# Performance work log

Measured on AMD Instinct MI355X. Metric: run time of the kernel, lower is better.

The kernel has to match this reference:

```python
import jax, jax.numpy as jnp
import numpy as np

N, E, G = 50000, 800000, 512
DIN, H, DOUT, L = 128, 256, 128, 5
H4 = 4 * H


def _ffnn(h, W1, b1, W2, b2):
    # Linear -> exact GELU (torch default) -> Linear
    return jax.nn.gelu(h @ W1 + b1, approximate=False) @ W2 + b2


def _mean_pool(h, batch):
    s = jax.ops.segment_sum(h, batch, num_segments=G)
    c = jax.ops.segment_sum(jnp.ones((h.shape[0], 1), h.dtype), batch, num_segments=G)
    return s / jnp.maximum(c, 1.0)


def setup_inputs() -> dict:
    key = jax.random.key(0)
    ks = iter(jax.random.split(key, 64))
    w = lambda *s: jax.random.normal(next(ks), s, jnp.float32) * 0.02
    z = lambda *s: jnp.zeros(s, jnp.float32)
    inp = {
        'x': jax.random.normal(next(ks), (N, DIN), jnp.float32),
        'edge_index': jax.random.randint(next(ks), (2, E), 0, N, jnp.int32),
        'batch': jnp.sort(jax.random.randint(next(ks), (N,), 0, G, jnp.int32)),
        'pre_W1': w(DIN, H), 'pre_b1': z(H), 'pre_W2': w(H, H), 'pre_b2': z(H),
        'gin_W1': w(L, H, H), 'gin_b1': z(L, H), 'gin_W2': w(L, H, H), 'gin_b2': z(L, H),
        'ffn_W1': w(L, H, H), 'ffn_b1': z(L, H), 'ffn_W2': w(L, H, H), 'ffn_b2': z(L, H),
        'upd_W1': w(L, H, H), 'upd_b1': z(L, H), 'upd_W2': w(L, H, H4), 'upd_b2': z(L, H4),
        'prop_W1': w(L, H4, H), 'prop_b1': z(L, H), 'prop_W2': w(L, H, H), 'prop_b2': z(L, H),
        'bn_gamma': jnp.ones((L, H), jnp.float32), 'bn_beta': z(L, H),
        'vn': jax.random.normal(next(ks), (1, H4), jnp.float32),
        'post_W1': w(H, H), 'post_b1': z(H), 'post_W2': w(H, DOUT), 'post_b2': z(DOUT),
    }
    return inp


def reference(x, edge_index, batch,
              pre_W1, pre_b1, pre_W2, pre_b2,
              gin_W1, gin_b1, gin_W2, gin_b2,
              ffn_W1, ffn_b1, ffn_W2, ffn_b2,
              upd_W1, upd_b1, upd_W2, upd_b2,
              prop_W1, prop_b1, prop_W2, prop_b2,
              bn_gamma, bn_beta, vn,
              post_W1, post_b1, post_W2, post_b2):
    src, dst = edge_index[0], edge_index[1]
    h = _ffnn(x, pre_W1, pre_b1, pre_W2, pre_b2)
    for i in range(L):
        # virtual node update and propagation
        v = vn + _ffnn(_mean_pool(h, batch), upd_W1[i], upd_b1[i], upd_W2[i], upd_b2[i])  # [G, 4H]
        outvn = _ffnn(v, prop_W1[i], prop_b1[i], prop_W2[i], prop_b2[i])  # [G, H]
        # GINConv (eps=0): nn((1+eps)*h + sum_{j->i} h_j), residual
        agg = jax.ops.segment_sum(h[src], dst, num_segments=N)
        h = _ffnn(h + agg, gin_W1[i], gin_b1[i], gin_W2[i], gin_b2[i]) + h
        # BatchNorm1d (batch statistics, biased var)
        mu = jnp.mean(h, axis=0)
        var = jnp.mean((h - mu) ** 2, axis=0)
        h = (h - mu) * jax.lax.rsqrt(var + 1e-5) * bn_gamma[i] + bn_beta[i]
        # broadcast VN to nodes, FFNN with residual (dropout = identity in eval)
        h = _ffnn(outvn[batch] + h, ffn_W1[i], ffn_b1[i], ffn_W2[i], ffn_b2[i]) + h
    out = _ffnn(_mean_pool(h, batch), post_W1, post_b1, post_W2, post_b2)
    return out
```

## Files before the change

### kernel.cpp

```cpp
#include <hip/hip_runtime.h>
#include <hip/hip_bf16.h>
#include <math.h>

#define NN 50000
#define NNP 50048
#define NE 800000
#define NG 512
#define DIN 128
#define HD 256
#define DOUT 128
#define NL 5
#define H4 1024

typedef _Float16 f16x8 __attribute__((ext_vector_type(8)));
typedef _Float16 f16x4 __attribute__((ext_vector_type(4)));
typedef float f32x4 __attribute__((ext_vector_type(4)));

__device__ __forceinline__ float gelu_exact(float x) {
    return 0.5f * x * (1.0f + erff(x * 0.70710678118654752f));
}

__device__ __forceinline__ void gl_lds16(const _Float16* g, _Float16* l) {
    __builtin_amdgcn_global_load_lds(
        (const __attribute__((address_space(1))) unsigned int*)g,
        (__attribute__((address_space(3))) unsigned int*)l, 16, 0, 0);
}

__global__ void k_hist(const int* __restrict__ idx, int* __restrict__ cnt, int n) {
    int i = blockIdx.x * blockDim.x + threadIdx.x;
    if (i < n) atomicAdd(&cnt[idx[i]], 1);
}

__global__ void k_scan_small(const int* __restrict__ in, int* __restrict__ out, int n) {
    __shared__ int buf[1024];
    int t = threadIdx.x;
    int v = (t < n) ? in[t] : 0;
    buf[t] = v;
    __syncthreads();
    for (int off = 1; off < 1024; off <<= 1) {
        int x = (t >= off) ? buf[t - off] : 0;
        __syncthreads();
        buf[t] += x;
        __syncthreads();
    }
    if (t < n) out[t] = buf[t] - v;
    if (t == 1023) out[n] = buf[1023];
}

__global__ void k_scan_part(const int* __restrict__ in, int* __restrict__ bsum, int n) {
    __shared__ int buf[256];
    int i = blockIdx.x * 256 + threadIdx.x;
    buf[threadIdx.x] = (i < n) ? in[i] : 0;
    __syncthreads();
    for (int off = 128; off > 0; off >>= 1) {
        if (threadIdx.x < off) buf[threadIdx.x] += buf[threadIdx.x + off];
        __syncthreads();
    }
    if (threadIdx.x == 0) bsum[blockIdx.x] = buf[0];
}

__global__ void k_scan_mid(const int* __restrict__ bsum, int* __restrict__ bexcl, int nb,
                           int* __restrict__ out, int n) {
    __shared__ int buf[1024];
    int t = threadIdx.x;
    int v = (t < nb) ? bsum[t] : 0;
    buf[t] = v;
    __syncthreads();
    for (int off = 1; off < 1024; off <<= 1) {
        int x = (t >= off) ? buf[t - off] : 0;
        __syncthreads();
        buf[t] += x;
        __syncthreads();
    }
    if (t < nb) bexcl[t] = buf[t] - v;
    if (t == 1023) out[n] = buf[1023];
}

__global__ void k_scan_out(const int* __restrict__ in, const int* __restrict__ bexcl,
                           int* __restrict__ out, int n) {
    __shared__ int buf[256];
    int i = blockIdx.x * 256 + threadIdx.x;
    int t = threadIdx.x;
    int v = (i < n) ? in[i] : 0;
    buf[t] = v;
    __syncthreads();
    for (int off = 1; off < 256; off <<= 1) {
        int x = (t >= off) ? buf[t - off] : 0;
        __syncthreads();
        buf[t] += x;
        __syncthreads();
    }
    if (i < n) out[i] = bexcl[blockIdx.x] + buf[t] - v;
}

__global__ void k_fill_csr(const int* __restrict__ src, const int* __restrict__ dst,
                           const int* __restrict__ eoff, int* __restrict__ cursor,
                           int* __restrict__ csr, int n) {
    int e = blockIdx.x * blockDim.x + threadIdx.x;
    if (e < n) {
        int d = dst[e];
        int p = atomicAdd(&cursor[d], 1);
        csr[eoff[d] + p] = src[e];
    }
}

__global__ void k_cvt16(const float* __restrict__ in, _Float16* __restrict__ out, int n4) {
    int i = blockIdx.x * blockDim.x + threadIdx.x;
    if (i < n4) {
        float4 v = *(const float4*)&in[i * 4];
        f16x4 o = { (_Float16)v.x, (_Float16)v.y, (_Float16)v.z, (_Float16)v.w };
        *(f16x4*)&out[i * 4] = o;
    }
}

#define NWTJOBS 44
struct WtJobs {
    const float* src[NWTJOBS];
    _Float16* dst[NWTJOBS];
    short K32[NWTJOBS];
    short N32[NWTJOBS];
    short pre[NWTJOBS + 1];
};
__global__ void k_wtb(WtJobs j) {
    int bid = blockIdx.x;
    int lo = 0;
    while (j.pre[lo + 1] <= bid) ++lo;
    int tl = bid - j.pre[lo];
    int nx = j.N32[lo];
    int n0 = (tl % nx) * 32, k0 = (tl / nx) * 32;
    int K = j.K32[lo] * 32, N = nx * 32;
    const float* W = j.src[lo];
    _Float16* Wt = j.dst[lo];
    __shared__ float tile[32][33];
    for (int i = threadIdx.y; i < 32; i += 8)
        tile[i][threadIdx.x] = W[(size_t)(k0 + i) * N + n0 + threadIdx.x];
    __syncthreads();
    for (int i = threadIdx.y; i < 32; i += 8)
        Wt[(size_t)(n0 + i) * K + k0 + threadIdx.x] = (_Float16)tile[threadIdx.x][i];
}

__global__ void k_pool16(const _Float16* __restrict__ h16, const int* __restrict__ goff,
                         _Float16* __restrict__ pool) {
    int g = blockIdx.x;
    int c = threadIdx.x;
    int s = goff[g], e = goff[g + 1];
    float acc = 0.f;
    for (int r = s; r < e; ++r) acc += (float)h16[(size_t)r * HD + c];
    int cnt = e - s;
    pool[g * HD + c] = (_Float16)(acc / (float)(cnt > 0 ? cnt : 1));
}

__global__ __launch_bounds__(256) void k_agg16(const _Float16* __restrict__ h16,
                                               const int* __restrict__ eoff,
                                               const int* __restrict__ csr,
                                               _Float16* __restrict__ out) {
    int node = blockIdx.x * 4 + (threadIdx.x >> 6);
    int lane = threadIdx.x & 63;
    int half = lane >> 5, l = lane & 31;
    f16x8 mine = *(const f16x8*)&h16[(size_t)node * HD + l * 8];
    float acc[8];
#pragma unroll
    for (int q = 0; q < 8; ++q) acc[q] = half ? 0.f : (float)mine[q];
    int s = eoff[node], e = eoff[node + 1];
    for (int base = s; base < e; base += 64) {
        int myi = base + lane;
        int vidx = (myi < e) ? csr[myi] : 0;
        int cnt = min(64, e - base);
        int jj = 0;
        for (; jj + 7 < cnt; jj += 8) {
            int s0 = __shfl(vidx, jj + half);
            int s1 = __shfl(vidx, jj + 2 + half);
            int s2 = __shfl(vidx, jj + 4 + half);
            int s3 = __shfl(vidx, jj + 6 + half);
            f16x8 v0 = *(const f16x8*)&h16[(size_t)s0 * HD + l * 8];
            f16x8 v1 = *(const f16x8*)&h16[(size_t)s1 * HD + l * 8];
            f16x8 v2 = *(const f16x8*)&h16[(size_t)s2 * HD + l * 8];
            f16x8 v3 = *(const f16x8*)&h16[(size_t)s3 * HD + l * 8];
#pragma unroll
            for (int q = 0; q < 8; ++q)
                acc[q] += ((float)v0[q] + (float)v1[q]) + ((float)v2[q] + (float)v3[q]);
        }
        for (; jj + 3 < cnt; jj += 4) {
            int s0 = __shfl(vidx, jj + half);
            int s1 = __shfl(vidx, jj + 2 + half);
            f16x8 v0 = *(const f16x8*)&h16[(size_t)s0 * HD + l * 8];
            f16x8 v1 = *(const f16x8*)&h16[(size_t)s1 * HD + l * 8];
#pragma unroll
            for (int q = 0; q < 8; ++q) acc[q] += (float)v0[q] + (float)v1[q];
        }
        for (; jj < cnt; jj += 2) {
            int i0 = jj + half;
            int s0 = __shfl(vidx, i0);
            if (i0 < cnt) {
                f16x8 v0 = *(const f16x8*)&h16[(size_t)s0 * HD + l * 8];
#pragma unroll
                for (int q = 0; q < 8; ++q) acc[q] += (float)v0[q];
            }
        }
    }
#pragma unroll
    for (int q = 0; q < 8; ++q) acc[q] += __shfl_xor(acc[q], 32);
    if (!half) {
        f16x8 o;
#pragma unroll
        for (int q = 0; q < 8; ++q) o[q] = (_Float16)acc[q];
        *(f16x8*)&out[(size_t)node * HD + l * 8] = o;
    }
}

__global__ void k_bn_final(float* __restrict__ stat,
                           const float* __restrict__ gamma, const float* __restrict__ beta,
                           float* __restrict__ scale, float* __restrict__ shift) {
    int c = threadIdx.x;
    float mu = stat[c] * (1.0f / NN);
    float var = stat[HD + c] * (1.0f / NN) - mu * mu;
    float rs = rsqrtf(var + 1e-5f);
    float sc = rs * gamma[c];
    scale[c] = sc;
    shift[c] = beta[c] - mu * sc;
    stat[c] = 0.f;
    stat[HD + c] = 0.f;
}

template <bool ABN1, bool RES2, bool RESBN2, bool STATS2>
__global__ __launch_bounds__(512) void k_b2b(const _Float16* __restrict__ A16,
                                             const _Float16* __restrict__ G16,
                                             const _Float16* __restrict__ W1t,
                                             const float* __restrict__ b1,
                                             const _Float16* __restrict__ W2t,
                                             const float* __restrict__ b2,
                                             const _Float16* __restrict__ R16,
                                             const float* __restrict__ bnsc,
                                             const float* __restrict__ bnsh,
                                             const float* __restrict__ ovn,
                                             const int* __restrict__ batchv,
                                             float* __restrict__ stat,
                                             _Float16* __restrict__ C16,
                                             int M, int K1) {
    __shared__ _Float16 AC[32][64][8];
    __shared__ _Float16 Bs[2][4][256][8];
    const int t = threadIdx.x;
    const int w = t >> 6, lane = t & 63;
    const int m0 = blockIdx.x * 64;
    const int kb = lane >> 4, fr = lane & 15, rr = lane >> 4;

    auto stageB = [&](int buf, int k0, const _Float16* Wt, int KB) {
        int s0 = t, s1 = t + 512;
        gl_lds16(Wt + (size_t)(s0 & 255) * KB + k0 + (s0 >> 8) * 8, &Bs[buf][s0 >> 8][s0 & 255][0]);
        gl_lds16(Wt + (size_t)(s1 & 255) * KB + k0 + (s1 >> 8) * 8, &Bs[buf][s1 >> 8][s1 & 255][0]);
    };

    const int nchunk = K1 * 8;
    if constexpr (ABN1) {
        for (int c = t; c < nchunk; c += 512) {
            int kblk = c >> 6, row = c & 63;
            int b0 = batchv[min(m0 + row, M - 1)];
            const int c0 = kblk * 8;
            f16x8 g = *(const f16x8*)&G16[(size_t)(m0 + row) * HD + c0];
            f16x8 r0;
#pragma unroll
            for (int q = 0; q < 8; ++q)
                r0[q] = (_Float16)((float)g[q] * bnsc[c0 + q] + bnsh[c0 + q] +
                                   ovn[(size_t)b0 * HD + c0 + q]);
            *(f16x8*)&AC[kblk][row][0] = r0;
        }
    } else {
        for (int c = t; c < nchunk; c += 512) {
            int kblk = c >> 6, row = c & 63;
            gl_lds16(A16 + (size_t)(m0 + row) * K1 + kblk * 8, &AC[kblk][row][0]);
        }
    }
    stageB(0, 0, W1t, K1);
    __syncthreads();

    f32x4 acc1[4][2];
#pragma unroll
    for (int mi = 0; mi < 4; ++mi)
#pragma unroll
        for (int ni = 0; ni < 2; ++ni) acc1[mi][ni] = (f32x4){0.f, 0.f, 0.f, 0.f};

    const int nt1 = K1 >> 5;
    for (int tt = 0; tt < nt1; ++tt) {
        const int cur = tt & 1;
        if (tt + 1 < nt1) stageB(cur ^ 1, (tt + 1) << 5, W1t, K1);
        f16x8 af[4], bf[2];
#pragma unroll
        for (int mi = 0; mi < 4; ++mi)
            af[mi] = *(const f16x8*)&AC[(tt << 2) + kb][mi * 16 + fr][0];
#pragma unroll
        for (int ni = 0; ni < 2; ++ni)
            bf[ni] = *(const f16x8*)&Bs[cur][kb][w * 32 + ni * 16 + fr][0];
#pragma unroll
        for (int mi = 0; mi < 4; ++mi)
#pragma unroll
            for (int ni = 0; ni < 2; ++ni)
                acc1[mi][ni] = __builtin_amdgcn_mfma_f32_16x16x32_f16(af[mi], bf[ni], acc1[mi][ni], 0, 0, 0);
        __syncthreads();
    }

    stageB(0, 0, W2t, HD);
#pragma unroll
    for (int mi = 0; mi < 4; ++mi) {
#pragma unroll
        for (int reg = 0; reg < 4; ++reg) {
            int ml = mi * 16 + rr * 4 + reg;
#pragma unroll
            for (int ni = 0; ni < 2; ++ni) {
                int n = w * 32 + ni * 16 + fr;
                float v = gelu_exact(acc1[mi][ni][reg] + b1[n]);
                AC[n >> 3][ml][n & 7] = (_Float16)v;
            }
        }
    }
    __syncthreads();

    f32x4 acc2[4][2];
#pragma unroll
    for (int mi = 0; mi < 4; ++mi)
#pragma unroll
        for (int ni = 0; ni < 2; ++ni) acc2[mi][ni] = (f32x4){0.f, 0.f, 0.f, 0.f};

    for (int tt = 0; tt < 8; ++tt) {
        const int cur = tt & 1;
        if (tt + 1 < 8) stageB(cur ^ 1, (tt + 1) << 5, W2t, HD);
        f16x8 af[4], bf[2];
#pragma unroll
        for (int mi = 0; mi < 4; ++mi)
            af[mi] = *(const f16x8*)&AC[tt * 4 + kb][mi * 16 + fr][0];
#pragma unroll
        for (int ni = 0; ni < 2; ++ni)
            bf[ni] = *(const f16x8*)&Bs[cur][kb][w * 32 + ni * 16 + fr][0];
#pragma unroll
        for (int mi = 0; mi < 4; ++mi)
#pragma unroll
            for (int ni = 0; ni < 2; ++ni)
                acc2[mi][ni] = __builtin_amdgcn_mfma_f32_16x16x32_f16(af[mi], bf[ni], acc2[mi][ni], 0, 0, 0);
        __syncthreads();
    }

    float cs[2] = {0.f, 0.f}, cq[2] = {0.f, 0.f};
#pragma unroll
    for (int mi = 0; mi < 4; ++mi) {
#pragma unroll
        for (int reg = 0; reg < 4; ++reg) {
            int m = m0 + mi * 16 + rr * 4 + reg;
            if (m < M) {
#pragma unroll
                for (int ni = 0; ni < 2; ++ni) {
                    int n = w * 32 + ni * 16 + fr;
                    float v = acc2[mi][ni][reg] + b2[n];
                    if (RES2) v += (float)R16[(size_t)m * HD + n];
                    if (RESBN2) v += (float)R16[(size_t)m * HD + n] * bnsc[n] + bnsh[n];
                    _Float16 vh = (_Float16)v;
                    C16[(size_t)m * HD + n] = vh;
                    if (STATS2) { float vr = (float)vh; cs[ni] += vr; cq[ni] += vr * vr; }
                }
            }
        }
    }
    if constexpr (STATS2) {
#pragma unroll
        for (int ni = 0; ni < 2; ++ni) {
            cs[ni] += __shfl_xor(cs[ni], 16); cs[ni] += __shfl_xor(cs[ni], 32);
            cq[ni] += __shfl_xor(cq[ni], 16); cq[ni] += __shfl_xor(cq[ni], 32);
        }
        if (lane < 16) {
#pragma unroll
            for (int ni = 0; ni < 2; ++ni) {
                int n = w * 32 + ni * 16 + lane;
                atomicAdd(&stat[n], cs[ni]);
                atomicAdd(&stat[HD + n], cq[ni]);
            }
        }
    }
}

template <bool GELU, bool BIAS2, bool O32, bool O16>
__global__ __launch_bounds__(256) void k_mgemm(const _Float16* __restrict__ A,
                                               const _Float16* __restrict__ Wt,
                                               const float* __restrict__ bias,
                                               const float* __restrict__ bias2,
                                               float* __restrict__ C32,
                                               _Float16* __restrict__ C16,
                                               int M, int N, int K) {
    __shared__ _Float16 As[2][4][64][8];
    __shared__ _Float16 Bs[2][4][128][8];
    const int t = threadIdx.x;
    const int w = t >> 6, lane = t & 63;
    const int m0 = blockIdx.y * 64, n0 = blockIdx.x * 128;
    const int kb = lane >> 4, fr = lane & 15;

    f32x4 acc[4][2];
#pragma unroll
    for (int mi = 0; mi < 4; ++mi)
#pragma unroll
        for (int ni = 0; ni < 2; ++ni) acc[mi][ni] = (f32x4){0.f, 0.f, 0.f, 0.f};

    const _Float16* gA0 = A + (size_t)(m0 + lane) * K + w * 8;
    const _Float16* gB0 = Wt + (size_t)(n0 + lane) * K + w * 8;
    const _Float16* gB1 = Wt + (size_t)(n0 + 64 + lane) * K + w * 8;

    auto stage = [&](int buf, int k0) {
        gl_lds16(gB0 + k0, &Bs[buf][w][0][0]);
        gl_lds16(gB1 + k0, &Bs[buf][w][64][0]);
        gl_lds16(gA0 + k0, &As[buf][w][0][0]);
    };

    const int nt = K >> 5;
    stage(0, 0);
    __syncthreads();
    for (int tt = 0; tt < nt; ++tt) {
        const int cur = tt & 1;
        if (tt + 1 < nt) stage(cur ^ 1, (tt + 1) << 5);
        f16x8 af[4], bf[2];
#pragma unroll
        for (int mi = 0; mi < 4; ++mi)
            af[mi] = *(const f16x8*)&As[cur][kb][mi * 16 + fr][0];
#pragma unroll
        for (int ni = 0; ni < 2; ++ni)
            bf[ni] = *(const f16x8*)&Bs[cur][kb][w * 32 + ni * 16 + fr][0];
#pragma unroll
        for (int mi = 0; mi < 4; ++mi)
#pragma unroll
            for (int ni = 0; ni < 2; ++ni)
                acc[mi][ni] = __builtin_amdgcn_mfma_f32_16x16x32_f16(af[mi], bf[ni], acc[mi][ni], 0, 0, 0);
        __syncthreads();
    }

    const int rr = lane >> 4;
#pragma unroll
    for (int mi = 0; mi < 4; ++mi) {
#pragma unroll
        for (int reg = 0; reg < 4; ++reg) {
            int m = m0 + mi * 16 + rr * 4 + reg;
            if (m < M) {
#pragma unroll
                for (int ni = 0; ni < 2; ++ni) {
                    int n = n0 + w * 32 + ni * 16 + fr;
                    float v = acc[mi][ni][reg] + bias[n];
                    if (BIAS2) v += bias2[n];
                    if (GELU) v = gelu_exact(v);
                    if (O32) C32[(size_t)m * N + n] = v;
                    if (O16) C16[(size_t)m * N + n] = (_Float16)v;
                }
            }
        }
    }
}

static inline void mg_gelu(hipStream_t st, const _Float16* A, const _Float16* Wt,
                           const float* bias, _Float16* C16, int M, int N, int K) {
    dim3 g(N / 128, (M + 63) / 64), b(256);
    k_mgemm<true, false, false, true><<<g, b, 0, st>>>(A, Wt, bias, nullptr, nullptr, C16, M, N, K);
}
static inline void mg_bias2_16(hipStream_t st, const _Float16* A, const _Float16* Wt,
                               const float* bias, const float* bias2, _Float16* C16,
                               int M, int N, int K) {
    dim3 g(N / 128, (M + 63) / 64), b(256);
    k_mgemm<false, true, false, true><<<g, b, 0, st>>>(A, Wt, bias, bias2, nullptr, C16, M, N, K);
}
static inline void mg_f32only(hipStream_t st, const _Float16* A, const _Float16* Wt,
                              const float* bias, float* C32, int M, int N, int K) {
    dim3 g(N / 128, (M + 63) / 64), b(256);
    k_mgemm<false, false, true, false><<<g, b, 0, st>>>(A, Wt, bias, nullptr, C32, nullptr, M, N, K);
}

extern "C" void kernel_launch(void* const* d_in, const int* in_sizes, int n_in,
                              void* d_out, int out_size, void* d_ws, size_t ws_size,
                              hipStream_t stream) {
    const float* x       = (const float*)d_in[0];
    const int*   ei      = (const int*)d_in[1];
    const int*   batch   = (const int*)d_in[2];
    const float* pre_W1  = (const float*)d_in[3];
    const float* pre_b1  = (const float*)d_in[4];
    const float* pre_W2  = (const float*)d_in[5];
    const float* pre_b2  = (const float*)d_in[6];
    const float* gin_W1  = (const float*)d_in[7];
    const float* gin_b1  = (const float*)d_in[8];
    const float* gin_W2  = (const float*)d_in[9];
    const float* gin_b2  = (const float*)d_in[10];
    const float* ffn_W1  = (const float*)d_in[11];
    const float* ffn_b1  = (const float*)d_in[12];
    const float* ffn_W2  = (const float*)d_in[13];
    const float* ffn_b2  = (const float*)d_in[14];
    const float* upd_W1  = (const float*)d_in[15];
    const float* upd_b1  = (const float*)d_in[16];
    const float* upd_W2  = (const float*)d_in[17];
    const float* upd_b2  = (const float*)d_in[18];
    const float* prop_W1 = (const float*)d_in[19];
    const float* prop_b1 = (const float*)d_in[20];
    const float* prop_W2 = (const float*)d_in[21];
    const float* prop_b2 = (const float*)d_in[22];
    const float* bn_gamma= (const float*)d_in[23];
    const float* bn_beta = (const float*)d_in[24];
    const float* vn      = (const float*)d_in[25];
    const float* post_W1 = (const float*)d_in[26];
    const float* post_b1 = (const float*)d_in[27];
    const float* post_W2 = (const float*)d_in[28];
    const float* post_b2 = (const float*)d_in[29];
    float* out = (float*)d_out;

    const int* e_src = ei;
    const int* e_dst = ei + NE;

    char* p = (char*)d_ws;
    auto alloc = [&](size_t bytes) -> char* {
        char* r = p;
        p += (bytes + 255) & ~(size_t)255;
        return r;
    };
    _Float16* h16    = (_Float16*)alloc((size_t)NNP * HD * 2);
    _Float16* g16    = (_Float16*)alloc((size_t)NNP * HD * 2);
    _Float16* t16a   = (_Float16*)alloc((size_t)NNP * HD * 2);
    _Float16* pool16 = (_Float16*)alloc((size_t)NG * HD * 2);
    _Float16* u16    = (_Float16*)alloc((size_t)NG * HD * 2);
    _Float16* vb16   = (_Float16*)alloc((size_t)NG * H4 * 2);
    _Float16* p16    = (_Float16*)alloc((size_t)NG * HD * 2);
    float*    outvn32= (float*)alloc((size_t)NG * HD * 4);
    float*    bnstat = (float*)alloc(2 * HD * 4);
    float*    bnscale= (float*)alloc(HD * 4);
    float*    bnshift= (float*)alloc(HD * 4);
    _Float16* preW1t = (_Float16*)alloc((size_t)HD * DIN * 2);
    _Float16* preW2t = (_Float16*)alloc((size_t)HD * HD * 2);
    _Float16* ginW1t = (_Float16*)alloc((size_t)NL * HD * HD * 2);
    _Float16* ginW2t = (_Float16*)alloc((size_t)NL * HD * HD * 2);
    _Float16* ffnW1t = (_Float16*)alloc((size_t)NL * HD * HD * 2);
    _Float16* ffnW2t = (_Float16*)alloc((size_t)NL * HD * HD * 2);
    _Float16* updW1t = (_Float16*)alloc((size_t)NL * HD * HD * 2);
    _Float16* updW2t = (_Float16*)alloc((size_t)NL * HD * H4 * 2);
    _Float16* propW1t= (_Float16*)alloc((size_t)NL * H4 * HD * 2);
    _Float16* propW2t= (_Float16*)alloc((size_t)NL * HD * HD * 2);
    _Float16* postW1t= (_Float16*)alloc((size_t)HD * HD * 2);
    _Float16* postW2t= (_Float16*)alloc((size_t)DOUT * HD * 2);
    int* gcount = (int*)alloc(NG * 4);
    int* goff   = (int*)alloc((NG + 1) * 4);
    int* deg    = (int*)alloc(NN * 4);
    int* eoff   = (int*)alloc((NN + 1) * 4);
    int* cursor = (int*)alloc(NN * 4);
    int* csr    = (int*)alloc((size_t)NE * 4);
    int* bsum   = (int*)alloc(1024 * 4);
    int* bexcl  = (int*)alloc(1024 * 4);
    _Float16* x16 = t16a;

    {
        size_t span = (size_t)((char*)(cursor + NN) - (char*)gcount);
        hipMemsetAsync(gcount, 0, span, stream);
        hipMemsetAsync(bnstat, 0, 2 * HD * 4, stream);
    }
    hipLaunchKernelGGL(k_hist, dim3((NN + 255) / 256), dim3(256), 0, stream, batch, gcount, NN);
    hipLaunchKernelGGL(k_hist, dim3((NE + 255) / 256), dim3(256), 0, stream, e_dst, deg, NE);
    hipLaunchKernelGGL(k_scan_small, dim3(1), dim3(1024), 0, stream, gcount, goff, NG);
    {
        int nbN = (NN + 255) / 256;
        hipLaunchKernelGGL(k_scan_part, dim3(nbN), dim3(256), 0, stream, deg, bsum, NN);
        hipLaunchKernelGGL(k_scan_mid, dim3(1), dim3(1024), 0, stream, bsum, bexcl, nbN, eoff, NN);
        hipLaunchKernelGGL(k_scan_out, dim3(nbN), dim3(256), 0, stream, deg, bexcl, eoff, NN);
    }
    hipLaunchKernelGGL(k_fill_csr, dim3((NE + 255) / 256), dim3(256), 0, stream, e_src, e_dst, eoff, cursor, csr, NE);

    {
        WtJobs j;
        int idx = 0, tiles = 0;
        auto add = [&](const float* s, _Float16* d, int K, int N) {
            j.src[idx] = s; j.dst[idx] = d;
            j.K32[idx] = (short)(K / 32); j.N32[idx] = (short)(N / 32);
            j.pre[idx] = (short)tiles;
            tiles += (K / 32) * (N / 32);
            ++idx;
        };
        add(pre_W1, preW1t, DIN, HD);
        add(pre_W2, preW2t, HD, HD);
        add(post_W1, postW1t, HD, HD);
        add(post_W2, postW2t, HD, DOUT);
        for (int i = 0; i < NL; ++i) {
            add(gin_W1 + (size_t)i * HD * HD, ginW1t + (size_t)i * HD * HD, HD, HD);
            add(gin_W2 + (size_t)i * HD * HD, ginW2t + (size_t)i * HD * HD, HD, HD);
            add(ffn_W1 + (size_t)i * HD * HD, ffnW1t + (size_t)i * HD * HD, HD, HD);
            add(ffn_W2 + (size_t)i * HD * HD, ffnW2t + (size_t)i * HD * HD, HD, HD);
            add(upd_W1 + (size_t)i * HD * HD, updW1t + (size_t)i * HD * HD, HD, HD);
            add(upd_W2 + (size_t)i * HD * H4, updW2t + (size_t)i * HD * H4, HD, H4);
            add(prop_W1 + (size_t)i * H4 * HD, propW1t + (size_t)i * H4 * HD, H4, HD);
            add(prop_W2 + (size_t)i * HD * HD, propW2t + (size_t)i * HD * HD, HD, HD);
        }
        j.pre[idx] = (short)tiles;
        hipLaunchKernelGGL(k_wtb, dim3(tiles), dim3(32, 8), 0, stream, j);
    }

    int n4 = NN * DIN / 4;
    hipLaunchKernelGGL(k_cvt16, dim3((n4 + 255) / 256), dim3(256), 0, stream, x, x16, n4);

    const int nb2b = NNP / 64;

    hipLaunchKernelGGL((k_b2b<false, false, false, false>), dim3(nb2b), dim3(512), 0, stream,
                       x16, nullptr, preW1t, pre_b1, preW2t, pre_b2,
                       nullptr, nullptr, nullptr, nullptr, nullptr, nullptr,
                       h16, NN, DIN);

    for (int i = 0; i < NL; ++i) {
        const _Float16* uW1 = updW1t + (size_t)i * HD * HD;
        const _Float16* uW2 = updW2t + (size_t)i * HD * H4;
        const _Float16* pW1 = propW1t + (size_t)i * H4 * HD;
        const _Float16* pW2 = propW2t + (size_t)i * HD * HD;

        hipLaunchKernelGGL(k_pool16, dim3(NG), dim3(HD), 0, stream, h16, goff, pool16);
        mg_gelu(stream, pool16, uW1, upd_b1 + (size_t)i * HD, u16, NG, HD, HD);
        mg_bias2_16(stream, u16, uW2, upd_b2 + (size_t)i * H4, vn, vb16, NG, H4, HD);
        mg_gelu(stream, vb16, pW1, prop_b1 + (size_t)i * HD, p16, NG, HD, H4);
        mg_f32only(stream, p16, pW2, prop_b2 + (size_t)i * HD, outvn32, NG, HD, HD);

        hipLaunchKernelGGL(k_agg16, dim3(NN / 4), dim3(256), 0, stream, h16, eoff, csr, t16a);
        hipLaunchKernelGGL((k_b2b<false, true, false, true>), dim3(nb2b), dim3(512), 0, stream,
                           t16a, nullptr,
                           ginW1t + (size_t)i * HD * HD, gin_b1 + (size_t)i * HD,
                           ginW2t + (size_t)i * HD * HD, gin_b2 + (size_t)i * HD,
                           h16, nullptr, nullptr, nullptr, nullptr, bnstat,
                           g16, NN, HD);

        hipLaunchKernelGGL(k_bn_final, dim3(1), dim3(HD), 0, stream, bnstat,
                           bn_gamma + (size_t)i * HD, bn_beta + (size_t)i * HD, bnscale, bnshift);

        hipLaunchKernelGGL((k_b2b<true, false, true, false>), dim3(nb2b), dim3(512), 0, stream,
                           nullptr, g16,
                           ffnW1t + (size_t)i * HD * HD, ffn_b1 + (size_t)i * HD,
                           ffnW2t + (size_t)i * HD * HD, ffn_b2 + (size_t)i * HD,
                           g16, bnscale, bnshift, outvn32, batch, nullptr,
                           h16, NN, HD);
    }

    hipLaunchKernelGGL(k_pool16, dim3(NG), dim3(HD), 0, stream, h16, goff, pool16);
    mg_gelu(stream, pool16, postW1t, post_b1, u16, NG, HD, HD);
    mg_f32only(stream, u16, postW2t, post_b2, out, NG, DOUT, HD);
}
```

Baseline: 1.674 ms.

## Triple-buffer weight staging across both GEMMs with one barrier per step

```diff
diff --git a/kernel.cpp b/kernel.cpp
--- a/kernel.cpp
+++ b/kernel.cpp
@@ -222,7 +222,7 @@
     stat[HD + c] = 0.f;
 }
 
-template <bool ABN1, bool RES2, bool RESBN2, bool STATS2>
+template <bool ABN1, bool RES2, bool RESBN2, bool STATS2, int K1>
 __global__ __launch_bounds__(512) void k_b2b(const _Float16* __restrict__ A16,
                                              const _Float16* __restrict__ G16,
                                              const _Float16* __restrict__ W1t,
@@ -236,23 +236,32 @@
                                              const int* __restrict__ batchv,
                                              float* __restrict__ stat,
                                              _Float16* __restrict__ C16,
-                                             int M, int K1) {
+                                             int M) {
     __shared__ _Float16 AC[32][64][8];
-    __shared__ _Float16 Bs[2][4][256][8];
+    __shared__ _Float16 Bs[3][4][256][8];
+    constexpr int NT1 = K1 >> 5;
+    constexpr int NSTEP = NT1 + 8;
     const int t = threadIdx.x;
     const int w = t >> 6, lane = t & 63;
     const int m0 = blockIdx.x * 64;
     const int kb = lane >> 4, fr = lane & 15, rr = lane >> 4;
 
-    auto stageB = [&](int buf, int k0, const _Float16* Wt, int KB) {
+    auto stageB = [&](int s) {
+        const _Float16* Wt = (s < NT1) ? W1t : W2t;
+        const int KB = (s < NT1) ? K1 : HD;
+        const int k0 = ((s < NT1) ? s : (s - NT1)) << 5;
+        const int buf = s % 3;
         int s0 = t, s1 = t + 512;
         gl_lds16(Wt + (size_t)(s0 & 255) * KB + k0 + (s0 >> 8) * 8, &Bs[buf][s0 >> 8][s0 & 255][0]);
         gl_lds16(Wt + (size_t)(s1 & 255) * KB + k0 + (s1 >> 8) * 8, &Bs[buf][s1 >> 8][s1 & 255][0]);
     };
 
-    const int nchunk = K1 * 8;
+    float b1r[2];
+#pragma unroll
+    for (int ni = 0; ni < 2; ++ni) b1r[ni] = b1[w * 32 + ni * 16 + fr];
+
     if constexpr (ABN1) {
-        for (int c = t; c < nchunk; c += 512) {
+        for (int c = t; c < K1 * 8; c += 512) {
             int kblk = c >> 6, row = c & 63;
             int b0 = batchv[min(m0 + row, M - 1)];
             const int c0 = kblk * 8;
@@ -265,13 +274,15 @@
             *(f16x8*)&AC[kblk][row][0] = r0;
         }
     } else {
-        for (int c = t; c < nchunk; c += 512) {
+        for (int c = t; c < K1 * 8; c += 512) {
             int kblk = c >> 6, row = c & 63;
             gl_lds16(A16 + (size_t)(m0 + row) * K1 + kblk * 8, &AC[kblk][row][0]);
         }
     }
-    stageB(0, 0, W1t, K1);
-    __syncthreads();
+    stageB(0);
+    stageB(1);
+    asm volatile("s_waitcnt vmcnt(2) lgkmcnt(0)" ::: "memory");
+    __builtin_amdgcn_s_barrier();
 
     f32x4 acc1[4][2];
 #pragma unroll
@@ -279,26 +290,29 @@
 #pragma unroll
         for (int ni = 0; ni < 2; ++ni) acc1[mi][ni] = (f32x4){0.f, 0.f, 0.f, 0.f};
 
-    const int nt1 = K1 >> 5;
-    for (int tt = 0; tt < nt1; ++tt) {
-        const int cur = tt & 1;
-        if (tt + 1 < nt1) stageB(cur ^ 1, (tt + 1) << 5, W1t, K1);
+#pragma unroll
+    for (int s = 0; s < NT1; ++s) {
+        if (s) {
+            asm volatile("s_waitcnt vmcnt(2)" ::: "memory");
+            __builtin_amdgcn_s_barrier();
+        }
         f16x8 af[4], bf[2];
 #pragma unroll
         for (int mi = 0; mi < 4; ++mi)
-            af[mi] = *(const f16x8*)&AC[(tt << 2) + kb][mi * 16 + fr][0];
+            af[mi] = *(const f16x8*)&AC[(s << 2) + kb][mi * 16 + fr][0];
 #pragma unroll
         for (int ni = 0; ni < 2; ++ni)
-            bf[ni] = *(const f16x8*)&Bs[cur][kb][w * 32 + ni * 16 + fr][0];
+            bf[ni] = *(const f16x8*)&Bs[s % 3][kb][w * 32 + ni * 16 + fr][0];
+        stageB(s + 2);
 #pragma unroll
         for (int mi = 0; mi < 4; ++mi)
 #pragma unroll
             for (int ni = 0; ni < 2; ++ni)
                 acc1[mi][ni] = __builtin_amdgcn_mfma_f32_16x16x32_f16(af[mi], bf[ni], acc1[mi][ni], 0, 0, 0);
-        __syncthreads();
-    }
-
-    stageB(0, 0, W2t, HD);
+    }
+
+    asm volatile("s_waitcnt vmcnt(2)" ::: "memory");
+    __builtin_amdgcn_s_barrier();
 #pragma unroll
     for (int mi = 0; mi < 4; ++mi) {
 #pragma unroll
@@ -307,12 +321,13 @@
 #pragma unroll
             for (int ni = 0; ni < 2; ++ni) {
                 int n = w * 32 + ni * 16 + fr;
-                float v = gelu_exact(acc1[mi][ni][reg] + b1[n]);
+                float v = gelu_exact(acc1[mi][ni][reg] + b1r[ni]);
                 AC[n >> 3][ml][n & 7] = (_Float16)v;
             }
         }
     }
-    __syncthreads();
+    asm volatile("s_waitcnt lgkmcnt(0)" ::: "memory");
+    __builtin_amdgcn_s_barrier();
 
     f32x4 acc2[4][2];
 #pragma unroll
@@ -320,22 +335,27 @@
 #pragma unroll
         for (int ni = 0; ni < 2; ++ni) acc2[mi][ni] = (f32x4){0.f, 0.f, 0.f, 0.f};
 
-    for (int tt = 0; tt < 8; ++tt) {
-        const int cur = tt & 1;
-        if (tt + 1 < 8) stageB(cur ^ 1, (tt + 1) << 5, W2t, HD);
+#pragma unroll
+    for (int s2 = 0; s2 < 8; ++s2) {
+        const int s = NT1 + s2;
+        if (s2) {
+            if (s2 == 7) asm volatile("s_waitcnt vmcnt(0)" ::: "memory");
+            else asm volatile("s_waitcnt vmcnt(2)" ::: "memory");
+            __builtin_amdgcn_s_barrier();
+        }
         f16x8 af[4], bf[2];
 #pragma unroll
         for (int mi = 0; mi < 4; ++mi)
-            af[mi] = *(const f16x8*)&AC[tt * 4 + kb][mi * 16 + fr][0];
+            af[mi] = *(const f16x8*)&AC[s2 * 4 + kb][mi * 16 + fr][0];
 #pragma unroll
         for (int ni = 0; ni < 2; ++ni)
-            bf[ni] = *(const f16x8*)&Bs[cur][kb][w * 32 + ni * 16 + fr][0];
+            bf[ni] = *(const f16x8*)&Bs[s % 3][kb][w * 32 + ni * 16 + fr][0];
+        if (s + 2 < NSTEP) stageB(s + 2);
 #pragma unroll
         for (int mi = 0; mi < 4; ++mi)
 #pragma unroll
             for (int ni = 0; ni < 2; ++ni)
                 acc2[mi][ni] = __builtin_amdgcn_mfma_f32_16x16x32_f16(af[mi], bf[ni], acc2[mi][ni], 0, 0, 0);
-        __syncthreads();
     }
 
     float cs[2] = {0.f, 0.f}, cq[2] = {0.f, 0.f};
@@ -591,10 +611,10 @@
 
     const int nb2b = NNP / 64;
 
-    hipLaunchKernelGGL((k_b2b<false, false, false, false>), dim3(nb2b), dim3(512), 0, stream,
+    hipLaunchKernelGGL((k_b2b<false, false, false, false, DIN>), dim3(nb2b), dim3(512), 0, stream,
                        x16, nullptr, preW1t, pre_b1, preW2t, pre_b2,
                        nullptr, nullptr, nullptr, nullptr, nullptr, nullptr,
-                       h16, NN, DIN);
+                       h16, NN);
 
     for (int i = 0; i < NL; ++i) {
         const _Float16* uW1 = updW1t + (size_t)i * HD * HD;
@@ -609,22 +629,22 @@
         mg_f32only(stream, p16, pW2, prop_b2 + (size_t)i * HD, outvn32, NG, HD, HD);
 
         hipLaunchKernelGGL(k_agg16, dim3(NN / 4), dim3(256), 0, stream, h16, eoff, csr, t16a);
-        hipLaunchKernelGGL((k_b2b<false, true, false, true>), dim3(nb2b), dim3(512), 0, stream,
+        hipLaunchKernelGGL((k_b2b<false, true, false, true, HD>), dim3(nb2b), dim3(512), 0, stream,
                            t16a, nullptr,
                            ginW1t + (size_t)i * HD * HD, gin_b1 + (size_t)i * HD,
                            ginW2t + (size_t)i * HD * HD, gin_b2 + (size_t)i * HD,
                            h16, nullptr, nullptr, nullptr, nullptr, bnstat,
-                           g16, NN, HD);
+                           g16, NN);
 
         hipLaunchKernelGGL(k_bn_final, dim3(1), dim3(HD), 0, stream, bnstat,
                            bn_gamma + (size_t)i * HD, bn_beta + (size_t)i * HD, bnscale, bnshift);
 
-        hipLaunchKernelGGL((k_b2b<true, false, true, false>), dim3(nb2b), dim3(512), 0, stream,
+        hipLaunchKernelGGL((k_b2b<true, false, true, false, HD>), dim3(nb2b), dim3(512), 0, stream,
                            nullptr, g16,
                            ffnW1t + (size_t)i * HD * HD, ffn_b1 + (size_t)i * HD,
                            ffnW2t + (size_t)i * HD * HD, ffn_b2 + (size_t)i * HD,
                            g16, bnscale, bnshift, outvn32, batch, nullptr,
-                           h16, NN, HD);
+                           h16, NN);
     }
 
     hipLaunchKernelGGL(k_pool16, dim3(NG), dim3(HD), 0, stream, h16, goff, pool16);
```

Measured after the change: 1.648 ms. No clear change (-1.6%).
